# Kernel tuning notes

Hardware: AMD Instinct MI355X
Metric: run time of the kernel (lower is better)

The kernel has to match this reference:

```python
import jax, jax.numpy as jnp
import numpy as np

B, S, D, C, I = 2, 1024, 1024, 64, 2048
N = S // C            # num_chunks (S divisible by C -> no padding)
EPS = 1e-6
BASE_LR = 0.01


def setup_inputs() -> dict:
    key = jax.random.key(0)
    ks = jax.random.split(key, 12)
    def xavier(k, shape):
        fan_in = shape[-1]
        return jax.random.normal(k, shape, jnp.float32) * (1.0 / np.sqrt(fan_in))
    return {
        "x": jax.random.normal(ks[0], (B, S, D), jnp.float32),
        "w1": xavier(ks[1], (I, D)),          # memory layer 0 weight [out,in]
        "w2": xavier(ks[2], (D, I)),          # memory layer 1 weight
        "ln_w": jnp.ones((D,), jnp.float32),  # memory RMSNorm weight
        "wq": xavier(ks[3], (D, D)),
        "wk": xavier(ks[4], (D, D)),
        "wv": xavier(ks[5], (D, D)),
        "qn_w": jnp.ones((D,), jnp.float32),
        "kn_w": jnp.ones((D,), jnp.float32),
        "alpha_w": jax.random.normal(ks[6], (1, C * D), jnp.float32) * 1e-3,
        "theta_w": jax.random.normal(ks[7], (1, C * D), jnp.float32) * 1e-3,
        "eta_w": jax.random.normal(ks[8], (1, C * D), jnp.float32) * 1e-3,
    }


def _rms(x, w):
    return x * jax.lax.rsqrt(jnp.mean(x * x, axis=-1, keepdims=True) + EPS) * w


def _memory_fwd(params, x):
    # 2-layer MLP memory with RMSNorm + residual
    w1, w2, lnw = params
    h = jax.nn.silu(x @ w1.T)
    y = h @ w2.T
    return x + _rms(y, lnw)


def _comb(e1, e2):
    # binary_operator: (a_j*a_i, kv_j + a_j*kv_i)
    a_i, kv_i = e1
    a_j, kv_j = e2
    return (a_j * a_i, kv_j + a_j * kv_i)


def _assocscan_update(pm, ps, g, eta, alpha):
    # pm,ps: [B,*s], g: [B,N,*s], eta/alpha: [B,N]
    extra = g.ndim - 2
    e = eta.reshape(eta.shape + (1,) * extra)
    a = alpha.reshape(alpha.shape + (1,) * extra)
    ones = jnp.ones_like(e[:, :1])
    # surprise recurrence: S_t = eta_t * S_{t-1} - g_t
    cS = jnp.concatenate([ones, e], axis=1)
    vS = jnp.concatenate([ps[:, None], -g], axis=1)
    _, Ssec = jax.lax.associative_scan(_comb, (cS, vS), axis=1)
    # memory recurrence: M_t = (1-alpha_t) * M_{t-1} + S_t
    cM = jnp.concatenate([ones, 1.0 - a], axis=1)
    vM = jnp.concatenate([pm[:, None], Ssec[:, 1:]], axis=1)
    _, Msec = jax.lax.associative_scan(_comb, (cM, vM), axis=1)
    return Msec[:, -1], Ssec[:, -1]


def reference(x, w1, w2, ln_w, wq, wk, wv, qn_w, kn_w, alpha_w, theta_w, eta_w):
    x4 = x.reshape(B, N, C, D)
    xc = x4.reshape(B, N, C * D)
    alpha = jax.nn.sigmoid(xc @ alpha_w.T)[..., 0]           # [B,N]
    theta = jax.nn.sigmoid(xc @ theta_w.T) * BASE_LR         # [B,N,1]
    eta = jax.nn.sigmoid(xc @ eta_w.T)[..., 0]               # [B,N]

    k = _rms(jax.nn.silu(x4 @ wk.T), kn_w)                   # [B,N,C,D]
    v = jax.nn.silu(x4 @ wv.T)                               # [B,N,C,D]

    # batched memory params (get_memory_params expands over batch)
    bw1 = jnp.broadcast_to(w1, (B,) + w1.shape)
    bw2 = jnp.broadcast_to(w2, (B,) + w2.shape)
    bln = jnp.broadcast_to(ln_w, (B,) + ln_w.shape)
    # initial surprises = 0
    s1 = jnp.zeros_like(bw1)
    s2 = jnp.zeros_like(bw2)
    sl = jnp.zeros_like(bln)

    def loss(p, ki, vi, th):
        pred = _memory_fwd(p, ki)
        return jnp.sum(jnp.mean((vi - pred) ** 2 * th, axis=-1))

    per_sample_grad = jax.vmap(jax.vmap(jax.grad(loss), in_axes=(None, 0, 0, 0)),
                               in_axes=(0, 0, 0, 0))
    g1, g2, gl = per_sample_grad((bw1, bw2, bln), k, v, theta)  # [B,N,*param]

    nw1, ns1 = _assocscan_update(bw1, s1, g1, eta, alpha)
    nw2, ns2 = _assocscan_update(bw2, s2, g2, eta, alpha)
    nln, nsl = _assocscan_update(bln, sl, gl, eta, alpha)

    # retrieve with updated memory
    q = _rms(jax.nn.silu(x4 @ wq.T), qn_w)                   # [B,N,C,D]
    out = jax.vmap(_memory_fwd)((nw1, nw2, nln), q)          # [B,N,C,D]
    out = out.reshape(B, S, D)
    return (out, nw1, nw2, nln, ns1, ns2, nsl)
```

## Files before the change

kernel.cpp:

```cpp
#include <hip/hip_runtime.h>

#define KD 1024
#define KI 2048
#define KB 2
#define KS 1024
#define KC 64
#define KN 16
#define KEPS 1e-6f

typedef __bf16 bf16x8 __attribute__((ext_vector_type(8)));
typedef __bf16 bf16x4 __attribute__((ext_vector_type(4)));
typedef float f32x4 __attribute__((ext_vector_type(4)));

__device__ __forceinline__ float sigf(float x){ return 1.0f/(1.0f+__expf(-x)); }
__device__ __forceinline__ float siluf(float x){ return x*sigf(x); }
__device__ __forceinline__ float dsiluf(float x){ float s=sigf(x); return s*(1.0f+x*(1.0f-s)); }

__device__ __forceinline__ void gld16(const __bf16* g, __bf16* l) {
  __builtin_amdgcn_global_load_lds(
    (const __attribute__((address_space(1))) unsigned int*)g,
    (__attribute__((address_space(3))) unsigned int*)l, 16, 0, 0);
}

#define WAIT_VM6()  asm volatile("s_waitcnt vmcnt(6)" ::: "memory")
#define WAIT_VM0()  asm volatile("s_waitcnt vmcnt(0)" ::: "memory")
#define WAIT_LGKM() asm volatile("s_waitcnt lgkmcnt(0)" ::: "memory")
#define BAR()       __builtin_amdgcn_s_barrier()

template<int SRCF>
__device__ __forceinline__ void tconv_body(const void* in, __bf16* out,
                                           int R, int Cc, int bx, int by)
{
  __shared__ float T[64][65];
  const int r0 = by*64, c0 = bx*64;
  const int tx = threadIdx.x & 15, ty = threadIdx.x >> 4;
  #pragma unroll
  for (int i=0;i<4;i++){
    const int r = r0 + ty + i*16;
    if (SRCF) {
      const float4 v = *(const float4*)((const float*)in + (size_t)r*Cc + c0 + tx*4);
      T[ty+i*16][tx*4+0]=v.x; T[ty+i*16][tx*4+1]=v.y;
      T[ty+i*16][tx*4+2]=v.z; T[ty+i*16][tx*4+3]=v.w;
    } else {
      const bf16x4 v = *(const bf16x4*)((const __bf16*)in + (size_t)r*Cc + c0 + tx*4);
      T[ty+i*16][tx*4+0]=(float)v[0]; T[ty+i*16][tx*4+1]=(float)v[1];
      T[ty+i*16][tx*4+2]=(float)v[2]; T[ty+i*16][tx*4+3]=(float)v[3];
    }
  }
  __syncthreads();
  #pragma unroll
  for (int i=0;i<4;i++){
    bf16x4 o = { (__bf16)T[tx*4+0][ty+i*16], (__bf16)T[tx*4+1][ty+i*16],
                 (__bf16)T[tx*4+2][ty+i*16], (__bf16)T[tx*4+3][ty+i*16] };
    *(bf16x4*)(out + (size_t)(c0+ty+i*16)*R + r0 + tx*4) = o;
  }
}

__global__ __launch_bounds__(256) void prep_kernel(
  const float* __restrict__ x, const float* __restrict__ wk, const float* __restrict__ wv,
  const float* __restrict__ wq, const float* __restrict__ w1, const float* __restrict__ w2,
  const float* __restrict__ aw, const float* __restrict__ tw, const float* __restrict__ ew,
  __bf16* __restrict__ xb, __bf16* __restrict__ wkb, __bf16* __restrict__ wvb,
  __bf16* __restrict__ wqb, __bf16* __restrict__ w1b, __bf16* __restrict__ w2b,
  __bf16* __restrict__ w2tb, float* __restrict__ part, float* __restrict__ gl)
{
  const int g = blockIdx.x;
  if (g < 2048) {
    const int i = g*256 + threadIdx.x;
    const float4 xv = *(const float4*)(x + (size_t)i*4);
    bf16x4 o = { (__bf16)xv.x, (__bf16)xv.y, (__bf16)xv.z, (__bf16)xv.w };
    *(bf16x4*)(xb + (size_t)i*4) = o;
    const size_t co = (size_t)(i & 16383) * 4;
    const float4 av = *(const float4*)(aw + co);
    const float4 tv = *(const float4*)(tw + co);
    const float4 ev = *(const float4*)(ew + co);
    float da = xv.x*av.x + xv.y*av.y + xv.z*av.z + xv.w*av.w;
    float dt = xv.x*tv.x + xv.y*tv.y + xv.z*tv.z + xv.w*tv.w;
    float de = xv.x*ev.x + xv.y*ev.y + xv.z*ev.z + xv.w*ev.w;
    __shared__ float sA[256], sT[256], sE[256];
    sA[threadIdx.x]=da; sT[threadIdx.x]=dt; sE[threadIdx.x]=de;
    __syncthreads();
    for (int s=128;s>0;s>>=1){
      if ((int)threadIdx.x < s){
        sA[threadIdx.x]+=sA[threadIdx.x+s];
        sT[threadIdx.x]+=sT[threadIdx.x+s];
        sE[threadIdx.x]+=sE[threadIdx.x+s];
      }
      __syncthreads();
    }
    if (threadIdx.x==0){
      part[g] = sA[0]; part[2048+g] = sT[0]; part[4096+g] = sE[0];
    }
  } else if (g < 9216) {
    const long t = (long)g*256 + threadIdx.x;
    const float* s; __bf16* d; long i;
    if (t < 786432)       { s=wk; d=wkb; i=t-524288; }
    else if (t < 1048576) { s=wv; d=wvb; i=t-786432; }
    else if (t < 1310720) { s=wq; d=wqb; i=t-1048576; }
    else if (t < 1835008) { s=w1; d=w1b; i=t-1310720; }
    else                  { s=w2; d=w2b; i=t-1835008; }
    const float4 v = *(const float4*)(s + i*4);
    bf16x4 o = { (__bf16)v.x, (__bf16)v.y, (__bf16)v.z, (__bf16)v.w };
    *(bf16x4*)(d + i*4) = o;
  } else if (g < 9728) {
    const int gg = g - 9216;
    tconv_body<1>(w2, w2tb, 1024, 2048, gg & 31, gg >> 5);
  } else {
    const int gg = g - 9728;
    float4 z = {0.f,0.f,0.f,0.f};
    *(float4*)(gl + (size_t)gg*1024 + threadIdx.x*4) = z;
  }
}

template<int EPI, int MODE, int WT>
__global__ __launch_bounds__(256) void mgemm2(
    const __bf16* __restrict__ A, const __bf16* __restrict__ B0,
    const __bf16* __restrict__ B1, const __bf16* __restrict__ B2,
    float* __restrict__ F0, float* __restrict__ F1,
    __bf16* __restrict__ Oa, __bf16* __restrict__ Ob, const __bf16* __restrict__ Aux,
    __bf16* __restrict__ OT, int ldt,
    int M, int Nn, int lda, int ldb, long bstr)
{
  const int bz = blockIdx.z;
  const int n0 = blockIdx.x * 64;
  const int m0 = blockIdx.y * 128;
  const __bf16* Bp = B0;
  if (MODE==1) { if (bz==1) Bp=B1; else if (bz==2) Bp=B2; }
  float* F0p = F0;
  int koff0 = 0;
  if (MODE==2) { koff0 = bz << 10; }
  Bp += (size_t)(m0 >> 10) * (size_t)bstr;
  __shared__ __bf16 As[2*128*64];
  __shared__ __bf16 Bs[2*64*64];
  const int tid = threadIdx.x, wv = tid >> 6, lane = tid & 63;
  const int wm = (wv >> 1) << 6, wn = (wv & 1) << 5;
  const int fr = lane & 15, fg = lane >> 4;
  const int lr = lane >> 3, lc = lane & 7;
  const __bf16* asrc[4]; __bf16* adst[4];
  const __bf16* bsrc[2]; __bf16* bdst[2];
  #pragma unroll
  for (int i=0;i<4;i++){
    const int rowbase=(wv*4+i)*8, row=rowbase+lr;
    asrc[i] = A + (size_t)(m0+row)*lda + koff0 + ((lc^(row&7))<<3);
    adst[i] = As + rowbase*64;
  }
  #pragma unroll
  for (int i=0;i<2;i++){
    const int rowbase=(wv*2+i)*8, row=rowbase+lr;
    bsrc[i] = Bp + (size_t)(n0+row)*ldb + koff0 + ((lc^(row&7))<<3);
    bdst[i] = Bs + rowbase*64;
  }
  f32x4 acc[4][2] = {};
  #pragma unroll
  for (int i=0;i<4;i++) gld16(asrc[i], adst[i]);
  #pragma unroll
  for (int i=0;i<2;i++) gld16(bsrc[i], bdst[i]);
  WAIT_VM0();
  BAR();
  #pragma unroll 2
  for (int t=0;t<16;++t){
    const int p = t & 1;
    if (t < 15){
      const int ko = (t+1) << 6;
      const int q = p ^ 1;
      #pragma unroll
      for (int i=0;i<4;i++) gld16(asrc[i]+ko, adst[i]+q*8192);
      #pragma unroll
      for (int i=0;i<2;i++) gld16(bsrc[i]+ko, bdst[i]+q*4096);
      WAIT_VM6();
    } else {
      WAIT_VM0();
    }
    BAR();
    #pragma unroll
    for (int ks=0;ks<2;++ks){
      bf16x8 af[4], bfv[2];
      #pragma unroll
      for (int mi=0;mi<4;++mi){
        const int r = wm + mi*16 + fr;
        af[mi] = *(const bf16x8*)(As + p*8192 + r*64 + ((((ks<<2)+fg)^(r&7))<<3));
      }
      #pragma unroll
      for (int ni=0;ni<2;++ni){
        const int r = wn + ni*16 + fr;
        bfv[ni] = *(const bf16x8*)(Bs + p*4096 + r*64 + ((((ks<<2)+fg)^(r&7))<<3));
      }
      #pragma unroll
      for (int mi=0;mi<4;++mi)
        #pragma unroll
        for (int ni=0;ni<2;++ni)
          acc[mi][ni] = __builtin_amdgcn_mfma_f32_16x16x32_bf16(af[mi], bfv[ni], acc[mi][ni], 0,0,0);
    }
    WAIT_LGKM();
    BAR();
  }
  __bf16* T = As;
  #pragma unroll
  for (int mi=0;mi<4;++mi){
    #pragma unroll
    for (int ni=0;ni<2;++ni){
      bf16x4 tv;
      #pragma unroll
      for (int j=0;j<4;++j){
        const int m = m0 + wm + mi*16 + fg*4 + j;
        const int n = n0 + wn + ni*16 + fr;
        const size_t idx = (size_t)m * Nn + n;
        const float v = acc[mi][ni][j];
        float tval = 0.f;
        if (EPI==0) F0p[idx] = v;
        else if (EPI==2) { const float sv = siluf(v); Oa[idx]=(__bf16)sv; Ob[idx]=(__bf16)dsiluf(v); tval=sv; }
        else if (EPI==3) tval = v * (float)Aux[idx];
        else if (EPI==4) Oa[idx] = (__bf16)siluf(v);
        else if (EPI==5) {
          if (bz==0) F0[idx] = siluf(v);
          else if (bz==1) Oa[idx] = (__bf16)siluf(v);
          else F1[idx] = siluf(v);
        }
        else if (EPI==6) Oa[(size_t)bz*M*Nn + idx] = (__bf16)v;
        if (WT) tv[j] = (__bf16)tval;
      }
      if (WT){
        const int nl = wn + ni*16 + fr;
        const int ml = wm + mi*16 + fg*4;
        *(bf16x4*)(T + nl*128 + (ml ^ ((nl&7)<<3))) = tv;
      }
    }
  }
  if (WT){
    __syncthreads();
    const int tn = tid >> 2, tc = tid & 3;
    #pragma unroll
    for (int u=0;u<4;++u){
      const int m8 = tc*32 + u*8;
      const bf16x8 v = *(const bf16x8*)(T + tn*128 + (m8 ^ ((tn&7)<<3)));
      *(bf16x8*)(OT + (size_t)(n0+tn)*ldt + m0 + m8) = v;
    }
  }
}

__device__ __forceinline__ void wacc_body(
    __bf16* As, __bf16* Bs,
    const __bf16* __restrict__ A, const __bf16* __restrict__ B,
    const float* __restrict__ Winit,
    const float* __restrict__ cm, const float* __restrict__ cs,
    const float* __restrict__ Pw,
    float* __restrict__ outM, __bf16* __restrict__ outMb, float* __restrict__ outS,
    int M, int Nn, int lda, int ldb, int n0, int m0, int bz)
{
  const int koff0 = bz << 10;
  const int tid = threadIdx.x, wv = tid >> 6, lane = tid & 63;
  const int wm = (wv >> 1) << 6, wn = (wv & 1) << 5;
  const int fr = lane & 15, fg = lane >> 4;
  const int lr = lane >> 3, lc = lane & 7;
  float cmr[KN], csr[KN];
  #pragma unroll
  for (int n=0;n<KN;n++){ cmr[n]=cm[bz*KN+n]; csr[n]=cs[bz*KN+n]; }
  const __bf16* asrc[4]; __bf16* adst[4];
  const __bf16* bsrc[2]; __bf16* bdst[2];
  #pragma unroll
  for (int i=0;i<4;i++){
    const int rowbase=(wv*4+i)*8, row=rowbase+lr;
    asrc[i] = A + (size_t)(m0+row)*lda + koff0 + ((lc^(row&7))<<3);
    adst[i] = As + rowbase*64;
  }
  #pragma unroll
  for (int i=0;i<2;i++){
    const int rowbase=(wv*2+i)*8, row=rowbase+lr;
    bsrc[i] = B + (size_t)(n0+row)*ldb + koff0 + ((lc^(row&7))<<3);
    bdst[i] = Bs + rowbase*64;
  }
  f32x4 accM[4][2] = {}, accS[4][2] = {};
  asm volatile("s_waitcnt vmcnt(0) lgkmcnt(0)" ::: "memory");
  #pragma unroll
  for (int i=0;i<4;i++) gld16(asrc[i], adst[i]);
  #pragma unroll
  for (int i=0;i<2;i++) gld16(bsrc[i], bdst[i]);
  WAIT_VM0();
  BAR();
  #pragma unroll 2
  for (int t=0;t<16;++t){
    const int p = t & 1;
    const float cmc = cmr[t], csc = csr[t];
    if (t < 15){
      const int ko = (t+1) << 6;
      const int q = p ^ 1;
      #pragma unroll
      for (int i=0;i<4;i++) gld16(asrc[i]+ko, adst[i]+q*8192);
      #pragma unroll
      for (int i=0;i<2;i++) gld16(bsrc[i]+ko, bdst[i]+q*4096);
      WAIT_VM6();
    } else {
      WAIT_VM0();
    }
    BAR();
    bf16x8 a0[4], a1[4], b0[2], b1[2];
    #pragma unroll
    for (int mi=0;mi<4;++mi){
      const int r = wm + mi*16 + fr;
      a0[mi] = *(const bf16x8*)(As + p*8192 + r*64 + (((0+fg)^(r&7))<<3));
      a1[mi] = *(const bf16x8*)(As + p*8192 + r*64 + (((4+fg)^(r&7))<<3));
    }
    #pragma unroll
    for (int ni=0;ni<2;++ni){
      const int r = wn + ni*16 + fr;
      b0[ni] = *(const bf16x8*)(Bs + p*4096 + r*64 + (((0+fg)^(r&7))<<3));
      b1[ni] = *(const bf16x8*)(Bs + p*4096 + r*64 + (((4+fg)^(r&7))<<3));
    }
    #pragma unroll
    for (int mi=0;mi<4;++mi){
      #pragma unroll
      for (int ni=0;ni<2;++ni){
        const f32x4 zf = {0.f,0.f,0.f,0.f};
        f32x4 P = __builtin_amdgcn_mfma_f32_16x16x32_bf16(a0[mi], b0[ni], zf, 0,0,0);
        P = __builtin_amdgcn_mfma_f32_16x16x32_bf16(a1[mi], b1[ni], P, 0,0,0);
        accM[mi][ni] += P * cmc;
        accS[mi][ni] += P * csc;
      }
    }
    WAIT_LGKM();
    BAR();
  }
  const float pw = Pw[bz];
  #pragma unroll
  for (int mi=0;mi<4;++mi){
    #pragma unroll
    for (int ni=0;ni<2;++ni){
      #pragma unroll
      for (int j=0;j<4;++j){
        const int m = m0 + wm + mi*16 + fg*4 + j;
        const int n = n0 + wn + ni*16 + fr;
        const size_t widx = (size_t)m * Nn + n;
        const size_t oidx = (size_t)bz * M * Nn + widx;
        const float vm = pw * Winit[widx] + accM[mi][ni][j];
        outM[oidx] = vm;
        outMb[oidx] = (__bf16)vm;
        outS[oidx] = accS[mi][ni][j];
      }
    }
  }
}

__global__ __launch_bounds__(256) void waccall_kernel(
    const __bf16* __restrict__ gaT, const __bf16* __restrict__ kT, const float* __restrict__ w1,
    const __bf16* __restrict__ gyT, const __bf16* __restrict__ hT, const float* __restrict__ w2,
    const float* __restrict__ gl, const float* __restrict__ lnw,
    const float* __restrict__ cm, const float* __restrict__ cs, const float* __restrict__ Pw,
    float* __restrict__ nw1, __bf16* __restrict__ nw1b, float* __restrict__ ns1,
    float* __restrict__ nw2, __bf16* __restrict__ nw2b, float* __restrict__ ns2,
    float* __restrict__ nln, float* __restrict__ nsl)
{
  __shared__ __bf16 As[2*128*64];
  __shared__ __bf16 Bs[2*64*64];
  const int g = blockIdx.x;
  if (g < 512){
    const int bz = g >> 8, rem = g & 255;
    wacc_body(As, Bs, gaT, kT, w1, cm, cs, Pw, nw1, nw1b, ns1,
              2048, 1024, 2048, 2048, (rem & 15)*64, (rem >> 4)*128, bz);
  } else if (g < 1024){
    const int t = g - 512;
    const int bz = t >> 8, rem = t & 255;
    wacc_body(As, Bs, gyT, hT, w2, cm, cs, Pw, nw2, nw2b, ns2,
              1024, 2048, 2048, 2048, (rem & 31)*64, (rem >> 5)*128, bz);
  } else {
    const int idx = (g - 1024)*256 + threadIdx.x;
    const int b = idx >> 10, d = idx & (KD-1);
    float am=0.f, as=0.f;
    for (int n=0;n<KN;n++){
      const float gv = gl[(size_t)(b*KN+n)*KD + d];
      am += cm[b*KN+n]*gv; as += cs[b*KN+n]*gv;
    }
    nln[idx] = Pw[b]*lnw[d] + am;
    nsl[idx] = as;
  }
}

__global__ __launch_bounds__(256) void rmsfuse_kernel(
    const float* __restrict__ kv, const float* __restrict__ kw, __bf16* __restrict__ k16,
    const float* __restrict__ qv, const float* __restrict__ qw, __bf16* __restrict__ q16,
    const float* __restrict__ part, float* __restrict__ cm, float* __restrict__ cs,
    float* __restrict__ Pw, float* __restrict__ theta)
{
  if (blockIdx.y == 2){
    if (blockIdx.x != 0) return;
    __shared__ float P[32][8][3];
    const int bn = threadIdx.x >> 3, sg = threadIdx.x & 7;
    float s0=0.f, s1=0.f, s2=0.f;
    #pragma unroll
    for (int u=0;u<8;u++){
      const int seg = bn*64 + sg*8 + u;
      s0 += part[seg]; s1 += part[2048+seg]; s2 += part[4096+seg];
    }
    P[bn][sg][0]=s0; P[bn][sg][1]=s1; P[bn][sg][2]=s2;
    __syncthreads();
    if ((int)threadIdx.x < KB){
      const int b = threadIdx.x;
      float al[KN], et[KN];
      for (int n=0;n<KN;n++){
        const int c = b*KN+n;
        float sa=0.f, st=0.f, se=0.f;
        #pragma unroll
        for (int k=0;k<8;k++){ sa+=P[c][k][0]; st+=P[c][k][1]; se+=P[c][k][2]; }
        al[n]=sigf(sa); theta[c]=sigf(st)*0.01f; et[n]=sigf(se);
      }
      float prodE = 1.f;
      for (int j=KN-1;j>=0;j--){ cs[b*KN+j] = -prodE; prodE *= et[j]; }
      float Ac[KN]; Ac[KN-1]=1.f;
      for (int t=KN-2;t>=0;t--) Ac[t] = Ac[t+1]*(1.f-al[t+1]);
      for (int j=0;j<KN;j++){
        float inner=0.f, E=1.f;
        for (int t=j;t<KN;t++){ inner += Ac[t]*E; if (t+1<KN) E *= et[t+1]; }
        cm[b*KN+j] = -inner;
      }
      float pw=1.f;
      for (int n=0;n<KN;n++) pw *= (1.f-al[n]);
      Pw[b]=pw;
    }
    return;
  }
  const float* v; const float* w; __bf16* o16;
  if (blockIdx.y == 0){ v=kv; w=kw; o16=k16; } else { v=qv; w=qw; o16=q16; }
  const int row = blockIdx.x * 4 + (threadIdx.x >> 6);
  const int lane = threadIdx.x & 63;
  const float* p = v + (size_t)row * KD;
  __bf16* p16 = o16 + (size_t)row * KD;
  float vals[16]; float ss = 0.f;
  #pragma unroll
  for (int l=0;l<16;l++){ vals[l] = p[lane + (l<<6)]; ss += vals[l]*vals[l]; }
  #pragma unroll
  for (int o=32;o>0;o>>=1) ss += __shfl_xor(ss, o, 64);
  const float inv = rsqrtf(ss * (1.0f/KD) + KEPS);
  #pragma unroll
  for (int l=0;l<16;l++){
    const int d = lane + (l<<6);
    p16[d] = (__bf16)(vals[l]*inv*w[d]);
  }
}

__global__ __launch_bounds__(256) void rms_grad_kernel(
    const __bf16* __restrict__ y16,
    const __bf16* __restrict__ k16, const __bf16* __restrict__ v16,
    const float* __restrict__ lnw, const float* __restrict__ theta,
    __bf16* __restrict__ gy, float* __restrict__ gl)
{
  const int wv = threadIdx.x >> 6;
  const int row = blockIdx.x * 4 + wv;
  const int lane = threadIdx.x & 63;
  const int chunk = blockIdx.x >> 4;
  const float th2 = theta[chunk] * (2.0f / KD);
  const __bf16* yr0 = y16 + (size_t)row * KD;
  const __bf16* yr1 = y16 + 2097152 + (size_t)row * KD;
  const __bf16* kr = k16 + (size_t)row * KD;
  const __bf16* vr = v16 + (size_t)row * KD;
  float yv[16]; float ss = 0.f;
  #pragma unroll
  for (int l=0;l<16;l++){
    const int d = lane + (l<<6);
    yv[l] = (float)yr0[d] + (float)yr1[d]; ss += yv[l]*yv[l];
  }
  #pragma unroll
  for (int o=32;o>0;o>>=1) ss += __shfl_xor(ss, o, 64);
  const float inv = rsqrtf(ss * (1.0f/KD) + KEPS);
  float gzv[16]; float sdot = 0.f;
  #pragma unroll
  for (int l=0;l<16;l++){
    const int d = lane + (l<<6);
    const float gz = th2 * ((float)kr[d] + yv[l]*inv*lnw[d] - (float)vr[d]);
    gzv[l] = gz;
    sdot += gz * lnw[d] * yv[l];
  }
  #pragma unroll
  for (int o=32;o>0;o>>=1) sdot += __shfl_xor(sdot, o, 64);
  const float c3 = inv*inv*inv * (1.0f/KD) * sdot;
  __bf16* gyr = gy + (size_t)row * KD;
  __shared__ float L[4][KD];
  #pragma unroll
  for (int l=0;l<16;l++){
    const int d = lane + (l<<6);
    gyr[d] = (__bf16)(inv * lnw[d] * gzv[l] - c3 * yv[l]);
    L[wv][d] = gzv[l] * yv[l] * inv;
  }
  __syncthreads();
  if (wv == 0){
    float* glc = gl + (size_t)chunk * KD;
    #pragma unroll
    for (int l=0;l<16;l++){
      const int d = lane + (l<<6);
      atomicAdd(&glc[d], L[0][d]+L[1][d]+L[2][d]+L[3][d]);
    }
  }
}

__global__ __launch_bounds__(256) void tconv2_kernel(
    const __bf16* __restrict__ kb16, __bf16* __restrict__ kT,
    const __bf16* __restrict__ gyb,  __bf16* __restrict__ gyT)
{
  const int g = blockIdx.x;
  if (g < 512)  tconv_body<0>(kb16, kT, 2048, 1024, g & 15, g >> 4);
  else        { const int t = g - 512; tconv_body<0>(gyb, gyT, 2048, 1024, t & 15, t >> 4); }
}

__global__ __launch_bounds__(256) void final_out_kernel(
    const __bf16* __restrict__ q16, const __bf16* __restrict__ yq16,
    const float* __restrict__ nln, float* __restrict__ out)
{
  const int row = blockIdx.x * 4 + (threadIdx.x >> 6);
  const int lane = threadIdx.x & 63;
  const int b = row >> 10;
  float yv[16]; float ss = 0.f;
  #pragma unroll
  for (int l=0;l<16;l++){
    const int d = lane + (l<<6);
    yv[l] = (float)yq16[(size_t)row*KD + d] + (float)yq16[2097152 + (size_t)row*KD + d];
    ss += yv[l]*yv[l];
  }
  #pragma unroll
  for (int o=32;o>0;o>>=1) ss += __shfl_xor(ss, o, 64);
  const float inv = rsqrtf(ss * (1.0f/KD) + KEPS);
  #pragma unroll
  for (int l=0;l<16;l++){
    const int d = lane + (l<<6);
    out[(size_t)row*KD + d] = (float)q16[(size_t)row*KD + d] + yv[l]*inv*nln[b*KD + d];
  }
}

extern "C" void kernel_launch(void* const* d_in, const int* in_sizes, int n_in,
                              void* d_out, int out_size, void* d_ws, size_t ws_size,
                              hipStream_t stream)
{
  const float* x    = (const float*)d_in[0];
  const float* w1   = (const float*)d_in[1];
  const float* w2   = (const float*)d_in[2];
  const float* lnw  = (const float*)d_in[3];
  const float* wq   = (const float*)d_in[4];
  const float* wk   = (const float*)d_in[5];
  const float* wv   = (const float*)d_in[6];
  const float* qnw  = (const float*)d_in[7];
  const float* knw  = (const float*)d_in[8];
  const float* aw   = (const float*)d_in[9];
  const float* tw   = (const float*)d_in[10];
  const float* ew   = (const float*)d_in[11];

  float* out = (float*)d_out;
  float* nw1 = out + (size_t)KB*KS*KD;
  float* nw2 = nw1 + (size_t)KB*KI*KD;
  float* nln = nw2 + (size_t)KB*KD*KI;
  float* ns1 = nln + (size_t)KB*KD;
  float* ns2 = ns1 + (size_t)KB*KI*KD;
  float* nsl = ns2 + (size_t)KB*KD*KI;

  float* ws = (float*)d_ws;
  size_t o = 0;
  float* kbuf = ws+o; o += 2097152;
  float* qbuf = ws+o; o += 2097152;
  float* gl   = ws+o; o += 32768;
  float* part = ws+o; o += 6144;
  float* cmb  = ws+o; o += 32;
  float* csb  = ws+o; o += 32;
  float* Pwb  = ws+o; o += 32;
  float* thetab = ws+o; o += 32;
  __bf16* bb = (__bf16*)(ws + o);
  size_t p = 0;
  __bf16* xb   = bb+p; p += 2097152;
  __bf16* wkb  = bb+p; p += 1048576;
  __bf16* wvb  = bb+p; p += 1048576;
  __bf16* wqb  = bb+p; p += 1048576;
  __bf16* w1b  = bb+p; p += 2097152;
  __bf16* w2b  = bb+p; p += 2097152;
  __bf16* w2tb = bb+p; p += 2097152;
  __bf16* kb16 = bb+p; p += 2097152;
  __bf16* qb16 = bb+p; p += 2097152;
  __bf16* vb16 = bb+p; p += 2097152;
  __bf16* hb16 = bb+p; p += 4194304;
  __bf16* db16 = bb+p; p += 4194304;
  __bf16* hT   = bb+p; p += 4194304;
  __bf16* gaT  = bb+p; p += 4194304;
  __bf16* nw1b = bb+p; p += 4194304;
  __bf16* nw2b = bb+p; p += 4194304;
  __bf16* y16  = bb+p; p += 4194304;
  __bf16* gyT = xb;
  __bf16* kT  = wkb;
  __bf16* gyb = w1b;
  __bf16* hq16= w2b;

  dim3 blk(256);

  prep_kernel<<<9760, blk, 0, stream>>>(x, wk, wv, wq, w1, w2, aw, tw, ew,
      xb, wkb, wvb, wqb, w1b, w2b, w2tb, part, gl);
  mgemm2<5,1,0><<<dim3(16,16,3), blk, 0, stream>>>(xb, wkb, wvb, wqb,
      kbuf, qbuf, vb16, nullptr, nullptr, nullptr, 0, 2048, 1024, 1024, 1024, 0);
  rmsfuse_kernel<<<dim3(512,3), blk, 0, stream>>>(kbuf, knw, kb16, qbuf, qnw, qb16,
      part, cmb, csb, Pwb, thetab);
  mgemm2<2,0,1><<<dim3(32,16,1), blk, 0, stream>>>(kb16, w1b, nullptr, nullptr,
      nullptr, nullptr, hb16, db16, nullptr, hT, 2048, 2048, 2048, 1024, 1024, 0);
  mgemm2<6,2,0><<<dim3(16,16,2), blk, 0, stream>>>(hb16, w2b, nullptr, nullptr,
      nullptr, nullptr, y16, nullptr, nullptr, nullptr, 0, 2048, 1024, 2048, 2048, 0);
  rms_grad_kernel<<<512, blk, 0, stream>>>(y16, kb16, vb16, lnw, thetab, gyb, gl);
  tconv2_kernel<<<1024, blk, 0, stream>>>(kb16, kT, gyb, gyT);
  mgemm2<3,0,1><<<dim3(32,16,1), blk, 0, stream>>>(gyb, w2tb, nullptr, nullptr,
      nullptr, nullptr, nullptr, nullptr, db16, gaT, 2048, 2048, 2048, 1024, 1024, 0);
  waccall_kernel<<<1032, blk, 0, stream>>>(gaT, kT, w1, gyT, hT, w2, gl, lnw,
      cmb, csb, Pwb, nw1, nw1b, ns1, nw2, nw2b, ns2, nln, nsl);
  mgemm2<4,0,0><<<dim3(32,16,1), blk, 0, stream>>>(qb16, nw1b, nullptr, nullptr,
      nullptr, nullptr, hq16, nullptr, nullptr, nullptr, 0, 2048, 2048, 1024, 1024, (long)KI*KD);
  mgemm2<6,2,0><<<dim3(16,16,2), blk, 0, stream>>>(hq16, nw2b, nullptr, nullptr,
      nullptr, nullptr, y16, nullptr, nullptr, nullptr, 0, 2048, 1024, 2048, 2048, (long)KD*KI);
  final_out_kernel<<<512, blk, 0, stream>>>(qb16, y16, nln, out);
}
```

Before: 200.1 us.

## Enlarge GEMM tiles to 128x128 and fuse transposes into GEMM launches

The bf16 MFMA GEMM moves from a 128x64 block tile to 128x128, so each wave computes a 64x64 sub-tile with more MFMAs per LDS fragment load and fewer blocks per GEMM. The standalone transpose kernel is removed; the kb16 and gyb transposes now run as extra blocks in the same launch as the following GEMMs and reuse their shared memory. This cuts launch count and improves operand reuse, but raises register and LDS use per block and halves grid sizes, which lowers occupancy and wave count on a large-CU device.

```diff
diff --git a/kernel.cpp b/kernel.cpp
--- a/kernel.cpp
+++ b/kernel.cpp
@@ -22,14 +22,35 @@
     (__attribute__((address_space(3))) unsigned int*)l, 16, 0, 0);
 }
 
+#define WAIT_VM8()  asm volatile("s_waitcnt vmcnt(8)" ::: "memory")
 #define WAIT_VM6()  asm volatile("s_waitcnt vmcnt(6)" ::: "memory")
 #define WAIT_VM0()  asm volatile("s_waitcnt vmcnt(0)" ::: "memory")
 #define WAIT_LGKM() asm volatile("s_waitcnt lgkmcnt(0)" ::: "memory")
 #define BAR()       __builtin_amdgcn_s_barrier()
 
-template<int SRCF>
-__device__ __forceinline__ void tconv_body(const void* in, __bf16* out,
-                                           int R, int Cc, int bx, int by)
+__device__ __forceinline__ void tconv_bodyP(float* T, const __bf16* in, __bf16* out,
+                                            int R, int Cc, int bx, int by)
+{
+  const int r0 = by*64, c0 = bx*64;
+  const int tx = threadIdx.x & 15, ty = threadIdx.x >> 4;
+  #pragma unroll
+  for (int i=0;i<4;i++){
+    const int r = r0 + ty + i*16;
+    const bf16x4 v = *(const bf16x4*)(in + (size_t)r*Cc + c0 + tx*4);
+    T[(ty+i*16)*65 + tx*4+0]=(float)v[0]; T[(ty+i*16)*65 + tx*4+1]=(float)v[1];
+    T[(ty+i*16)*65 + tx*4+2]=(float)v[2]; T[(ty+i*16)*65 + tx*4+3]=(float)v[3];
+  }
+  __syncthreads();
+  #pragma unroll
+  for (int i=0;i<4;i++){
+    bf16x4 o = { (__bf16)T[(tx*4+0)*65 + ty+i*16], (__bf16)T[(tx*4+1)*65 + ty+i*16],
+                 (__bf16)T[(tx*4+2)*65 + ty+i*16], (__bf16)T[(tx*4+3)*65 + ty+i*16] };
+    *(bf16x4*)(out + (size_t)(c0+ty+i*16)*R + r0 + tx*4) = o;
+  }
+}
+
+__device__ __forceinline__ void tconv_bodyF(const float* in, __bf16* out,
+                                            int R, int Cc, int bx, int by)
 {
   __shared__ float T[64][65];
   const int r0 = by*64, c0 = bx*64;
@@ -37,15 +58,9 @@
   #pragma unroll
   for (int i=0;i<4;i++){
     const int r = r0 + ty + i*16;
-    if (SRCF) {
-      const float4 v = *(const float4*)((const float*)in + (size_t)r*Cc + c0 + tx*4);
-      T[ty+i*16][tx*4+0]=v.x; T[ty+i*16][tx*4+1]=v.y;
-      T[ty+i*16][tx*4+2]=v.z; T[ty+i*16][tx*4+3]=v.w;
-    } else {
-      const bf16x4 v = *(const bf16x4*)((const __bf16*)in + (size_t)r*Cc + c0 + tx*4);
-      T[ty+i*16][tx*4+0]=(float)v[0]; T[ty+i*16][tx*4+1]=(float)v[1];
-      T[ty+i*16][tx*4+2]=(float)v[2]; T[ty+i*16][tx*4+3]=(float)v[3];
-    }
+    const float4 v = *(const float4*)(in + (size_t)r*Cc + c0 + tx*4);
+    T[ty+i*16][tx*4+0]=v.x; T[ty+i*16][tx*4+1]=v.y;
+    T[ty+i*16][tx*4+2]=v.z; T[ty+i*16][tx*4+3]=v.w;
   }
   __syncthreads();
   #pragma unroll
@@ -104,7 +119,7 @@
     *(bf16x4*)(d + i*4) = o;
   } else if (g < 9728) {
     const int gg = g - 9216;
-    tconv_body<1>(w2, w2tb, 1024, 2048, gg & 31, gg >> 5);
+    tconv_bodyF(w2, w2tb, 1024, 2048, gg & 31, gg >> 5);
   } else {
     const int gg = g - 9728;
     float4 z = {0.f,0.f,0.f,0.f};
@@ -113,48 +128,43 @@
 }
 
 template<int EPI, int MODE, int WT>
-__global__ __launch_bounds__(256) void mgemm2(
+__device__ __forceinline__ void mgemm_body(
+    __bf16* As, __bf16* Bs,
     const __bf16* __restrict__ A, const __bf16* __restrict__ B0,
     const __bf16* __restrict__ B1, const __bf16* __restrict__ B2,
     float* __restrict__ F0, float* __restrict__ F1,
     __bf16* __restrict__ Oa, __bf16* __restrict__ Ob, const __bf16* __restrict__ Aux,
     __bf16* __restrict__ OT, int ldt,
-    int M, int Nn, int lda, int ldb, long bstr)
-{
-  const int bz = blockIdx.z;
-  const int n0 = blockIdx.x * 64;
-  const int m0 = blockIdx.y * 128;
+    int M, int Nn, int lda, int ldb, long bstr,
+    int bx, int by, int bz)
+{
+  const int n0 = bx * 128;
+  const int m0 = by * 128;
   const __bf16* Bp = B0;
   if (MODE==1) { if (bz==1) Bp=B1; else if (bz==2) Bp=B2; }
   float* F0p = F0;
   int koff0 = 0;
-  if (MODE==2) { koff0 = bz << 10; }
+  if (MODE==2) koff0 = bz << 10;
   Bp += (size_t)(m0 >> 10) * (size_t)bstr;
-  __shared__ __bf16 As[2*128*64];
-  __shared__ __bf16 Bs[2*64*64];
   const int tid = threadIdx.x, wv = tid >> 6, lane = tid & 63;
-  const int wm = (wv >> 1) << 6, wn = (wv & 1) << 5;
+  const int wm = (wv >> 1) << 6, wn = (wv & 1) << 6;
   const int fr = lane & 15, fg = lane >> 4;
   const int lr = lane >> 3, lc = lane & 7;
   const __bf16* asrc[4]; __bf16* adst[4];
-  const __bf16* bsrc[2]; __bf16* bdst[2];
+  const __bf16* bsrc[4]; __bf16* bdst[4];
   #pragma unroll
   for (int i=0;i<4;i++){
     const int rowbase=(wv*4+i)*8, row=rowbase+lr;
     asrc[i] = A + (size_t)(m0+row)*lda + koff0 + ((lc^(row&7))<<3);
     adst[i] = As + rowbase*64;
-  }
-  #pragma unroll
-  for (int i=0;i<2;i++){
-    const int rowbase=(wv*2+i)*8, row=rowbase+lr;
     bsrc[i] = Bp + (size_t)(n0+row)*ldb + koff0 + ((lc^(row&7))<<3);
     bdst[i] = Bs + rowbase*64;
   }
-  f32x4 acc[4][2] = {};
+  f32x4 acc[4][4] = {};
   #pragma unroll
   for (int i=0;i<4;i++) gld16(asrc[i], adst[i]);
   #pragma unroll
-  for (int i=0;i<2;i++) gld16(bsrc[i], bdst[i]);
+  for (int i=0;i<4;i++) gld16(bsrc[i], bdst[i]);
   WAIT_VM0();
   BAR();
   #pragma unroll 2
@@ -166,29 +176,29 @@
       #pragma unroll
       for (int i=0;i<4;i++) gld16(asrc[i]+ko, adst[i]+q*8192);
       #pragma unroll
-      for (int i=0;i<2;i++) gld16(bsrc[i]+ko, bdst[i]+q*4096);
-      WAIT_VM6();
+      for (int i=0;i<4;i++) gld16(bsrc[i]+ko, bdst[i]+q*8192);
+      WAIT_VM8();
     } else {
       WAIT_VM0();
     }
     BAR();
     #pragma unroll
     for (int ks=0;ks<2;++ks){
-      bf16x8 af[4], bfv[2];
+      bf16x8 af[4], bfv[4];
       #pragma unroll
       for (int mi=0;mi<4;++mi){
         const int r = wm + mi*16 + fr;
         af[mi] = *(const bf16x8*)(As + p*8192 + r*64 + ((((ks<<2)+fg)^(r&7))<<3));
       }
       #pragma unroll
-      for (int ni=0;ni<2;++ni){
+      for (int ni=0;ni<4;++ni){
         const int r = wn + ni*16 + fr;
-        bfv[ni] = *(const bf16x8*)(Bs + p*4096 + r*64 + ((((ks<<2)+fg)^(r&7))<<3));
+        bfv[ni] = *(const bf16x8*)(Bs + p*8192 + r*64 + ((((ks<<2)+fg)^(r&7))<<3));
       }
       #pragma unroll
       for (int mi=0;mi<4;++mi)
         #pragma unroll
-        for (int ni=0;ni<2;++ni)
+        for (int ni=0;ni<4;++ni)
           acc[mi][ni] = __builtin_amdgcn_mfma_f32_16x16x32_bf16(af[mi], bfv[ni], acc[mi][ni], 0,0,0);
     }
     WAIT_LGKM();
@@ -198,7 +208,7 @@
   #pragma unroll
   for (int mi=0;mi<4;++mi){
     #pragma unroll
-    for (int ni=0;ni<2;++ni){
+    for (int ni=0;ni<4;++ni){
       bf16x4 tv;
       #pragma unroll
       for (int j=0;j<4;++j){
@@ -228,13 +238,64 @@
   }
   if (WT){
     __syncthreads();
-    const int tn = tid >> 2, tc = tid & 3;
-    #pragma unroll
-    for (int u=0;u<4;++u){
-      const int m8 = tc*32 + u*8;
+    const int tn = tid >> 1, tc = tid & 1;
+    #pragma unroll
+    for (int u=0;u<8;++u){
+      const int m8 = (tc*8+u)*8;
       const bf16x8 v = *(const bf16x8*)(T + tn*128 + (m8 ^ ((tn&7)<<3)));
       *(bf16x8*)(OT + (size_t)(n0+tn)*ldt + m0 + m8) = v;
     }
+  }
+}
+
+template<int EPI, int MODE, int WT>
+__global__ __launch_bounds__(256) void mgemm3(
+    const __bf16* __restrict__ A, const __bf16* __restrict__ B0,
+    const __bf16* __restrict__ B1, const __bf16* __restrict__ B2,
+    float* __restrict__ F0, float* __restrict__ F1,
+    __bf16* __restrict__ Oa, __bf16* __restrict__ Ob, const __bf16* __restrict__ Aux,
+    __bf16* __restrict__ OT, int ldt,
+    int M, int Nn, int lda, int ldb, long bstr)
+{
+  __shared__ __bf16 As[2*128*64];
+  __shared__ __bf16 Bs[2*128*64];
+  mgemm_body<EPI,MODE,WT>(As, Bs, A, B0, B1, B2, F0, F1, Oa, Ob, Aux, OT, ldt,
+                          M, Nn, lda, ldb, bstr, blockIdx.x, blockIdx.y, blockIdx.z);
+}
+
+__global__ __launch_bounds__(256) void gemm_a_kernel(
+    const __bf16* __restrict__ kb16, const __bf16* __restrict__ w1b,
+    __bf16* __restrict__ hb16, __bf16* __restrict__ db16, __bf16* __restrict__ hT,
+    __bf16* __restrict__ kT)
+{
+  __shared__ __bf16 As[2*128*64];
+  __shared__ __bf16 Bs[2*128*64];
+  const int g = blockIdx.x;
+  if (g < 256)
+    mgemm_body<2,0,1>(As, Bs, kb16, w1b, nullptr, nullptr, nullptr, nullptr,
+                      hb16, db16, nullptr, hT, 2048, 2048, 2048, 1024, 1024, 0,
+                      g & 15, g >> 4, 0);
+  else {
+    const int t = g - 256;
+    tconv_bodyP((float*)As, kb16, kT, 2048, 1024, t & 15, t >> 4);
+  }
+}
+
+__global__ __launch_bounds__(256) void gemm_ga_kernel(
+    const __bf16* __restrict__ gyb, const __bf16* __restrict__ w2tb,
+    const __bf16* __restrict__ db16, __bf16* __restrict__ gaT,
+    __bf16* __restrict__ gyT)
+{
+  __shared__ __bf16 As[2*128*64];
+  __shared__ __bf16 Bs[2*128*64];
+  const int g = blockIdx.x;
+  if (g < 256)
+    mgemm_body<3,0,1>(As, Bs, gyb, w2tb, nullptr, nullptr, nullptr, nullptr,
+                      nullptr, nullptr, db16, gaT, 2048, 2048, 2048, 1024, 1024, 0,
+                      g & 15, g >> 4, 0);
+  else {
+    const int t = g - 256;
+    tconv_bodyP((float*)As, gyb, gyT, 2048, 1024, t & 15, t >> 4);
   }
 }
 
@@ -488,15 +549,6 @@
       atomicAdd(&glc[d], L[0][d]+L[1][d]+L[2][d]+L[3][d]);
     }
   }
-}
-
-__global__ __launch_bounds__(256) void tconv2_kernel(
-    const __bf16* __restrict__ kb16, __bf16* __restrict__ kT,
-    const __bf16* __restrict__ gyb,  __bf16* __restrict__ gyT)
-{
-  const int g = blockIdx.x;
-  if (g < 512)  tconv_body<0>(kb16, kT, 2048, 1024, g & 15, g >> 4);
-  else        { const int t = g - 512; tconv_body<0>(gyb, gyT, 2048, 1024, t & 15, t >> 4); }
 }
 
 __global__ __launch_bounds__(256) void final_out_kernel(
@@ -586,23 +638,20 @@
 
   prep_kernel<<<9760, blk, 0, stream>>>(x, wk, wv, wq, w1, w2, aw, tw, ew,
       xb, wkb, wvb, wqb, w1b, w2b, w2tb, part, gl);
-  mgemm2<5,1,0><<<dim3(16,16,3), blk, 0, stream>>>(xb, wkb, wvb, wqb,
+  mgemm3<5,1,0><<<dim3(8,16,3), blk, 0, stream>>>(xb, wkb, wvb, wqb,
       kbuf, qbuf, vb16, nullptr, nullptr, nullptr, 0, 2048, 1024, 1024, 1024, 0);
   rmsfuse_kernel<<<dim3(512,3), blk, 0, stream>>>(kbuf, knw, kb16, qbuf, qnw, qb16,
       part, cmb, csb, Pwb, thetab);
-  mgemm2<2,0,1><<<dim3(32,16,1), blk, 0, stream>>>(kb16, w1b, nullptr, nullptr,
-      nullptr, nullptr, hb16, db16, nullptr, hT, 2048, 2048, 2048, 1024, 1024, 0);
-  mgemm2<6,2,0><<<dim3(16,16,2), blk, 0, stream>>>(hb16, w2b, nullptr, nullptr,
+  gemm_a_kernel<<<768, blk, 0, stream>>>(kb16, w1b, hb16, db16, hT, kT);
+  mgemm3<6,2,0><<<dim3(8,16,2), blk, 0, stream>>>(hb16, w2b, nullptr, nullptr,
       nullptr, nullptr, y16, nullptr, nullptr, nullptr, 0, 2048, 1024, 2048, 2048, 0);
   rms_grad_kernel<<<512, blk, 0, stream>>>(y16, kb16, vb16, lnw, thetab, gyb, gl);
-  tconv2_kernel<<<1024, blk, 0, stream>>>(kb16, kT, gyb, gyT);
-  mgemm2<3,0,1><<<dim3(32,16,1), blk, 0, stream>>>(gyb, w2tb, nullptr, nullptr,
-      nullptr, nullptr, nullptr, nullptr, db16, gaT, 2048, 2048, 2048, 1024, 1024, 0);
+  gemm_ga_kernel<<<768, blk, 0, stream>>>(gyb, w2tb, db16, gaT, gyT);
   waccall_kernel<<<1032, blk, 0, stream>>>(gaT, kT, w1, gyT, hT, w2, gl, lnw,
       cmb, csb, Pwb, nw1, nw1b, ns1, nw2, nw2b, ns2, nln, nsl);
-  mgemm2<4,0,0><<<dim3(32,16,1), blk, 0, stream>>>(qb16, nw1b, nullptr, nullptr,
+  mgemm3<4,0,0><<<dim3(16,16,1), blk, 0, stream>>>(qb16, nw1b, nullptr, nullptr,
       nullptr, nullptr, hq16, nullptr, nullptr, nullptr, 0, 2048, 2048, 1024, 1024, (long)KI*KD);
-  mgemm2<6,2,0><<<dim3(16,16,2), blk, 0, stream>>>(hq16, nw2b, nullptr, nullptr,
+  mgemm3<6,2,0><<<dim3(8,16,2), blk, 0, stream>>>(hq16, nw2b, nullptr, nullptr,
       nullptr, nullptr, y16, nullptr, nullptr, nullptr, 0, 2048, 1024, 2048, 2048, (long)KD*KI);
   final_out_kernel<<<512, blk, 0, stream>>>(qb16, y16, nln, out);
 }
```

Result: slower. 231.6 us (+15.7%).
